# Kernel tuning notes

Hardware: AMD Instinct MI355X
Metric: run time of the kernel (lower is better)

Reference implementation:

```python
import math
import jax, jax.numpy as jnp
import numpy as np

B, L, S, H, E, D = 2, 2048, 2048, 16, 64, 64

def setup_inputs() -> dict:
    key = jax.random.key(0)
    k1, k2, k3, k4, k5 = jax.random.split(key, 5)
    return {
        "queries": jax.random.normal(k1, (B, L, H, E), dtype=jnp.float32),
        "keys": jax.random.normal(k2, (B, S, H, E), dtype=jnp.float32),
        "values": jax.random.normal(k3, (B, S, H, D), dtype=jnp.float32),
        "tau": jax.random.uniform(k4, (B, 1), dtype=jnp.float32),
        "delta": jax.random.normal(k5, (B, S), dtype=jnp.float32),
        "attn_mask": jnp.zeros((1,), dtype=jnp.bool_),
    }

def reference(queries, keys, values, tau, delta, attn_mask):
    # queries: [B,L,H,E], keys: [B,S,H,E], values: [B,S,H,D]
    # tau: [B,1] -> [B,1,1,1]; delta: [B,S] -> [B,1,1,S]
    # mask_flag=False, so attn_mask is unused. Dropout is identity at eval.
    E_ = queries.shape[-1]
    scale = 1.0 / math.sqrt(E_)
    scores = jnp.einsum('blhe,bshe->bhls', queries, keys)  # [B,H,L,S]
    scores = scores * tau[:, None, None, :]                # de-stationary scale
    scores = scores + delta[:, None, None, :]              # de-stationary shift
    A = jax.nn.softmax(scale * scores, axis=-1)            # [B,H,L,S]
    V = jnp.einsum('bhls,bshd->blhd', A, values)           # [B,L,H,D]
    return V
```

## Files before the change

### kernel.cpp

```cpp
#include <hip/hip_runtime.h>


#define Bb 2
#define Ll 2048
#define Ss 2048
#define Hh 16
#define Ee 64
#define Dd 64
#define KV 64

typedef _Float16 f16x8 __attribute__((ext_vector_type(8)));
typedef _Float16 f16x4 __attribute__((ext_vector_type(4)));
typedef __fp16 fp16x2 __attribute__((ext_vector_type(2)));
typedef float f32x4 __attribute__((ext_vector_type(4)));

union Pk2 { fp16x2 h; unsigned u; };
union PackU { unsigned u[4]; f16x8 v; };

#define GLDS(gp, lp) __builtin_amdgcn_global_load_lds( \
    (const __attribute__((address_space(1))) void*)(gp), \
    (__attribute__((address_space(3))) void*)(lp), 16, 0, 0)

__global__ __launch_bounds__(256)
void prepass_k(const float* __restrict__ K, _Float16* __restrict__ K16,
               const float* __restrict__ delta, float* __restrict__ delta2)
{
    const unsigned v = blockIdx.x * 256 + threadIdx.x;
    const unsigned e4 = v & 15;
    const unsigned h  = (v >> 4) & 15;
    const unsigned s  = (v >> 8) & (Ss - 1);
    const unsigned b  = v >> 19;
    const f32x4 src = ((const f32x4*)K)[v];
    f16x4 t;
    t[0] = (_Float16)src[0]; t[1] = (_Float16)src[1];
    t[2] = (_Float16)src[2]; t[3] = (_Float16)src[3];
    ((f16x4*)K16)[(((size_t)(b * Hh + h) * Ss + s) * 16) + e4] = t;
    if (v < (Bb * Ss) / 4) {
        f32x4 dd = ((const f32x4*)delta)[v];
        ((f32x4*)delta2)[v] = (f32x4){0.125f * dd[0], 0.125f * dd[1],
                                      0.125f * dd[2], 0.125f * dd[3]};
    }
}

__global__ __launch_bounds__(256)
void prepass_v(const float* __restrict__ V, _Float16* __restrict__ VT16)
{
    __shared__ _Float16 TL[64][66];
    const int tid  = threadIdx.x;
    const int wave = tid >> 6;
    const int lane = tid & 63;
    const int bh = blockIdx.y;
    const int b  = bh >> 4;
    const int h  = bh & 15;
    const int s0 = blockIdx.x * 64;

    #pragma unroll
    for (int rr = 0; rr < 16; ++rr) {
        const int row = wave * 16 + rr;
        TL[row][lane] = (_Float16)V[((size_t)(b * Ss + s0 + row) * Hh + h) * Dd + lane];
    }
    __syncthreads();
    const int d  = tid >> 2;
    const int sq = (tid & 3) * 16;
    union { _Float16 h[16]; f16x8 v[2]; } tmp;
    #pragma unroll
    for (int i = 0; i < 16; ++i) tmp.h[i] = TL[sq + i][d];
    f16x8* dp = (f16x8*)(VT16 + ((size_t)(b * Hh + h) * Dd + d) * Ss + s0 + sq);
    dp[0] = tmp.v[0];
    dp[1] = tmp.v[1];
}

__global__ __launch_bounds__(256)
void dsattn_fwd_v4(const float* __restrict__ Q, const _Float16* __restrict__ K16,
                   const _Float16* __restrict__ VT16, const float* __restrict__ tau,
                   const float* __restrict__ delta2, float* __restrict__ out)
{
    extern __shared__ __align__(16) unsigned char smem[];

    const int tid  = threadIdx.x;
    const int wave = tid >> 6;
    const int lane = tid & 63;
    const int lq   = lane & 15;
    const int g    = lane >> 4;

    const int bh = blockIdx.y;
    const int b  = bh >> 4;
    const int h  = bh & 15;
    const int q0 = blockIdx.x * 128;
    const int qw = q0 + wave * 32;

    const float alpha = 0.125f * tau[b];

    f16x8 aq[2][2];
    #pragma unroll
    for (int qg = 0; qg < 2; ++qg) {
        const float* qp = Q + (((size_t)b * Ll + qw + qg * 16 + lq) * Hh + h) * Ee;
        #pragma unroll
        for (int es = 0; es < 2; ++es) {
            const float* p = qp + es * 32 + g * 8;
            f16x8 t;
            #pragma unroll
            for (int j = 0; j < 8; ++j) t[j] = (_Float16)p[j];
            aq[qg][es] = t;
        }
    }

    f32x4 osum[2][4];
    #pragma unroll
    for (int qg = 0; qg < 2; ++qg)
        #pragma unroll
        for (int i = 0; i < 4; ++i) osum[qg][i] = (f32x4){0.f, 0.f, 0.f, 0.f};
    float m_run[2] = {-1e30f, -1e30f};
    float l_run[2] = {0.0f, 0.0f};

    const unsigned char* kb  = (const unsigned char*)(K16 + (size_t)(b * Hh + h) * Ss * Ee);
    const unsigned char* vtb = (const unsigned char*)(VT16 + (size_t)(b * Hh + h) * Dd * Ss);
    const float* d2b = delta2 + (size_t)b * Ss;

    const int row0  = tid >> 3;
    const int slotS = (tid & 7) ^ (row0 & 7);

    {
        unsigned char* kw = smem + wave * 1024;
        unsigned char* vw = smem + 8192 + wave * 1024;
        GLDS(kb + (size_t)row0 * 128 + slotS * 16,        kw);
        GLDS(kb + (size_t)(row0 + 32) * 128 + slotS * 16, kw + 4096);
        GLDS(vtb + (size_t)row0 * (Ss * 2) + slotS * 16,        vw);
        GLDS(vtb + (size_t)(row0 + 32) * (Ss * 2) + slotS * 16, vw + 4096);
    }
    f32x4 dcur[4], dnxt[4];
    #pragma unroll
    for (int t = 0; t < 4; ++t)
        dcur[t] = *(const f32x4*)(d2b + t * 16 + 4 * g);
    __syncthreads();

    const int srcA = lq + 32 * (g & 1);
    const int srcB = srcA + 16;
    const bool gh = (g >> 1);

    int cur = 0;
    for (int sb = 0; sb < Ss; sb += KV) {
        const int nb = (sb + KV < Ss);
        if (nb) {
            unsigned char* kw = smem + (cur ^ 1) * 16384 + wave * 1024;
            unsigned char* vw = kw + 8192;
            const int sn = sb + KV;
            GLDS(kb + (size_t)(sn + row0) * 128 + slotS * 16,        kw);
            GLDS(kb + (size_t)(sn + row0 + 32) * 128 + slotS * 16,   kw + 4096);
            GLDS(vtb + (size_t)row0 * (Ss * 2) + sn * 2 + slotS * 16,        vw);
            GLDS(vtb + (size_t)(row0 + 32) * (Ss * 2) + sn * 2 + slotS * 16, vw + 4096);
        }
        {
            const int sn = nb ? sb + KV : sb;
            #pragma unroll
            for (int t = 0; t < 4; ++t)
                dnxt[t] = *(const f32x4*)(d2b + sn + t * 16 + 4 * g);
        }

        const unsigned char* Ksm = smem + cur * 16384;
        const unsigned char* Vsm = Ksm + 8192;

        f32x4 c4[2][4];
        #pragma unroll
        for (int qg = 0; qg < 2; ++qg)
            #pragma unroll
            for (int t = 0; t < 4; ++t) c4[qg][t] = (f32x4){0.f, 0.f, 0.f, 0.f};
        __builtin_amdgcn_s_setprio(1);
        #pragma unroll
        for (int t = 0; t < 4; ++t) {
            const int srow = t * 16 + lq;
            #pragma unroll
            for (int es = 0; es < 2; ++es) {
                const int slot = (es * 4 + g) ^ (srow & 7);
                f16x8 ak = *(const f16x8*)(Ksm + srow * 128 + slot * 16);
                c4[0][t] = __builtin_amdgcn_mfma_f32_16x16x32_f16(ak, aq[0][es], c4[0][t], 0, 0, 0);
                c4[1][t] = __builtin_amdgcn_mfma_f32_16x16x32_f16(ak, aq[1][es], c4[1][t], 0, 0, 0);
            }
        }
        __builtin_amdgcn_s_setprio(0);

        PackU bp[2][2];
        #pragma unroll
        for (int qg = 0; qg < 2; ++qg) {
            float p[16];
            float tmax = -1e30f;
            #pragma unroll
            for (int t = 0; t < 4; ++t)
                #pragma unroll
                for (int j = 0; j < 4; ++j) {
                    float z = fmaf(alpha, c4[qg][t][j], dcur[t][j]);
                    p[t * 4 + j] = z;
                    tmax = fmaxf(tmax, z);
                }
            tmax = fmaxf(tmax, __shfl_xor(tmax, 16));
            tmax = fmaxf(tmax, __shfl_xor(tmax, 32));
            if (!__all(tmax <= m_run[qg] + 8.0f)) {
                const float m_new = fmaxf(m_run[qg], tmax);
                const float corr  = __expf(m_run[qg] - m_new);
                l_run[qg] *= corr;
                #pragma unroll
                for (int dt = 0; dt < 4; ++dt)
                    #pragma unroll
                    for (int j = 0; j < 4; ++j)
                        osum[qg][dt][j] *= corr;
                m_run[qg] = m_new;
            }
            float psum = 0.f;
            #pragma unroll
            for (int i = 0; i < 16; ++i) { p[i] = __expf(p[i] - m_run[qg]); psum += p[i]; }
            psum += __shfl_xor(psum, 16);
            psum += __shfl_xor(psum, 32);
            l_run[qg] += psum;

            unsigned pk[8];
            #pragma unroll
            for (int t = 0; t < 4; ++t) {
                Pk2 u0, u1;
                u0.h = __builtin_amdgcn_cvt_pkrtz(p[4 * t], p[4 * t + 1]);
                u1.h = __builtin_amdgcn_cvt_pkrtz(p[4 * t + 2], p[4 * t + 3]);
                pk[t * 2] = u0.u;
                pk[t * 2 + 1] = u1.u;
            }
            #pragma unroll
            for (int ks = 0; ks < 2; ++ks) {
                unsigned a0 = __shfl(pk[ks * 4 + 0], srcA), a1 = __shfl(pk[ks * 4 + 1], srcA);
                unsigned a2 = __shfl(pk[ks * 4 + 2], srcA), a3 = __shfl(pk[ks * 4 + 3], srcA);
                unsigned b0 = __shfl(pk[ks * 4 + 0], srcB), b1 = __shfl(pk[ks * 4 + 1], srcB);
                unsigned b2 = __shfl(pk[ks * 4 + 2], srcB), b3 = __shfl(pk[ks * 4 + 3], srcB);
                bp[qg][ks].u[0] = gh ? a2 : a0;
                bp[qg][ks].u[1] = gh ? a3 : a1;
                bp[qg][ks].u[2] = gh ? b2 : b0;
                bp[qg][ks].u[3] = gh ? b3 : b1;
            }
        }

        __builtin_amdgcn_s_setprio(1);
        #pragma unroll
        for (int ks = 0; ks < 2; ++ks)
            #pragma unroll
            for (int dt = 0; dt < 4; ++dt) {
                const int vrow = dt * 16 + lq;
                const int slot = (ks * 4 + g) ^ (vrow & 7);
                f16x8 av = *(const f16x8*)(Vsm + vrow * 128 + slot * 16);
                osum[0][dt] = __builtin_amdgcn_mfma_f32_16x16x32_f16(av, bp[0][ks].v, osum[0][dt], 0, 0, 0);
                osum[1][dt] = __builtin_amdgcn_mfma_f32_16x16x32_f16(av, bp[1][ks].v, osum[1][dt], 0, 0, 0);
            }
        __builtin_amdgcn_s_setprio(0);

        __syncthreads();
        cur ^= 1;
        #pragma unroll
        for (int t = 0; t < 4; ++t) dcur[t] = dnxt[t];
    }

    float (*Osm)[32][68] = (float (*)[32][68])smem;
    #pragma unroll
    for (int qg = 0; qg < 2; ++qg) {
        const float inv = 1.0f / l_run[qg];
        #pragma unroll
        for (int dt = 0; dt < 4; ++dt)
            #pragma unroll
            for (int j = 0; j < 4; ++j)
                Osm[wave][qg * 16 + lq][dt * 16 + 4 * g + j] = osum[qg][dt][j] * inv;
    }
    __syncthreads();
    {
        float* ob = out + (((size_t)b * Ll + qw) * Hh + h) * Dd;
        #pragma unroll
        for (int r = 0; r < 32; ++r)
            ob[(size_t)r * (Hh * Dd) + lane] = Osm[wave][r][lane];
    }
}

__global__ __launch_bounds__(256)
void dsattn_fwd(const float* __restrict__ Q, const float* __restrict__ K,
                const float* __restrict__ V, const float* __restrict__ tau,
                const float* __restrict__ delta, float* __restrict__ out)
{
    __shared__ __align__(16) unsigned char Ksm[32 * 128];
    __shared__ __align__(16) unsigned char VTsm[64 * 80];
    __shared__ float dsm[32];
    __shared__ float Osm[4][16][68];

    const int tid  = threadIdx.x;
    const int wave = tid >> 6;
    const int lane = tid & 63;
    const int lq   = lane & 15;
    const int g    = lane >> 4;

    const int bh = blockIdx.y;
    const int b  = bh >> 4;
    const int h  = bh & 15;
    const int q0 = blockIdx.x * 64;

    const float alpha = 0.125f * tau[b];

    f16x8 aq[2];
    {
        const float* qp = Q + (((long)b * Ll + q0 + wave * 16 + lq) * Hh + h) * Ee;
        #pragma unroll
        for (int es = 0; es < 2; ++es) {
            const float* p = qp + es * 32 + g * 8;
            f16x8 t;
            #pragma unroll
            for (int j = 0; j < 8; ++j) t[j] = (_Float16)p[j];
            aq[es] = t;
        }
    }

    f32x4 osum[4];
    #pragma unroll
    for (int i = 0; i < 4; ++i) osum[i] = (f32x4){0.f, 0.f, 0.f, 0.f};
    float m_run = -1e30f, l_run = 0.0f;

    const float* kb = K + ((long)b * Ss * Hh + h) * Ee;
    const float* vb = V + ((long)b * Ss * Hh + h) * Dd;
    const float* db = delta + (long)b * Ss;

    const int kr    = tid >> 3;
    const int kc    = (tid & 7) * 8;
    const int kslot = (((tid & 7) ^ (kr & 7)) * 16);
    const int vd    = tid & 63;
    const int vsh   = tid >> 6;

    for (int sb = 0; sb < Ss; sb += 32) {
        __syncthreads();
        {
            const float* src = kb + (long)(sb + kr) * (Hh * Ee) + kc;
            f16x8 t;
            #pragma unroll
            for (int j = 0; j < 8; ++j) t[j] = (_Float16)src[j];
            *(f16x8*)(Ksm + kr * 128 + kslot) = t;
        }
        {
            const float* src = vb + (long)(sb + vsh * 8) * (Hh * Dd) + vd;
            f16x8 t;
            #pragma unroll
            for (int j = 0; j < 8; ++j) t[j] = (_Float16)src[j * (Hh * Dd)];
            *(f16x8*)(VTsm + vd * 80 + vsh * 16) = t;
        }
        if (tid < 32) dsm[tid] = 0.125f * db[sb + tid];
        __syncthreads();

        float p[8];
        float tmax = -1e30f;
        #pragma unroll
        for (int t = 0; t < 2; ++t) {
            f32x4 c = (f32x4){0.f, 0.f, 0.f, 0.f};
            #pragma unroll
            for (int es = 0; es < 2; ++es) {
                const int srow = t * 16 + lq;
                const int slot = ((es * 4 + g) ^ (srow & 7)) * 16;
                f16x8 ak = *(const f16x8*)(Ksm + srow * 128 + slot);
                c = __builtin_amdgcn_mfma_f32_16x16x32_f16(ak, aq[es], c, 0, 0, 0);
            }
            #pragma unroll
            for (int j = 0; j < 4; ++j) {
                float z = alpha * c[j] + dsm[t * 16 + 4 * g + j];
                p[t * 4 + j] = z;
                tmax = fmaxf(tmax, z);
            }
        }
        tmax = fmaxf(tmax, __shfl_xor(tmax, 16));
        tmax = fmaxf(tmax, __shfl_xor(tmax, 32));
        const float m_new = fmaxf(m_run, tmax);
        const float corr  = __expf(m_run - m_new);
        float psum = 0.f;
        #pragma unroll
        for (int i = 0; i < 8; ++i) { p[i] = __expf(p[i] - m_new); psum += p[i]; }
        psum += __shfl_xor(psum, 16);
        psum += __shfl_xor(psum, 32);
        l_run = l_run * corr + psum;
        m_run = m_new;
        #pragma unroll
        for (int dt = 0; dt < 4; ++dt)
            #pragma unroll
            for (int j = 0; j < 4; ++j)
                osum[dt][j] *= corr;

        Pk2 u00, u01, u10, u11;
        u00.h = __builtin_amdgcn_cvt_pkrtz(p[0], p[1]);
        u01.h = __builtin_amdgcn_cvt_pkrtz(p[2], p[3]);
        u10.h = __builtin_amdgcn_cvt_pkrtz(p[4], p[5]);
        u11.h = __builtin_amdgcn_cvt_pkrtz(p[6], p[7]);
        const int srcA = lq + 32 * (g & 1);
        const int srcB = srcA + 16;
        unsigned a00 = __shfl(u00.u, srcA), a01 = __shfl(u01.u, srcA);
        unsigned a10 = __shfl(u10.u, srcA), a11 = __shfl(u11.u, srcA);
        unsigned b00 = __shfl(u00.u, srcB), b01 = __shfl(u01.u, srcB);
        unsigned b10 = __shfl(u10.u, srcB), b11 = __shfl(u11.u, srcB);
        const bool hi = (g >= 2);
        PackU bp;
        bp.u[0] = hi ? a10 : a00;
        bp.u[1] = hi ? a11 : a01;
        bp.u[2] = hi ? b10 : b00;
        bp.u[3] = hi ? b11 : b01;

        #pragma unroll
        for (int dt = 0; dt < 4; ++dt) {
            f16x8 av = *(const f16x8*)(VTsm + (dt * 16 + lq) * 80 + g * 16);
            osum[dt] = __builtin_amdgcn_mfma_f32_16x16x32_f16(av, bp.v, osum[dt], 0, 0, 0);
        }
    }

    const float inv = 1.0f / l_run;
    #pragma unroll
    for (int dt = 0; dt < 4; ++dt)
        #pragma unroll
        for (int j = 0; j < 4; ++j)
            Osm[wave][lq][dt * 16 + 4 * g + j] = osum[dt][j] * inv;
    __syncthreads();
    {
        float* ob = out + (((long)b * Ll + q0 + wave * 16) * Hh + h) * Dd;
        #pragma unroll
        for (int r = 0; r < 16; ++r)
            ob[(long)r * (Hh * Dd) + lane] = Osm[wave][r][lane];
    }
}

extern "C" void kernel_launch(void* const* d_in, const int* in_sizes, int n_in,
                              void* d_out, int out_size, void* d_ws, size_t ws_size,
                              hipStream_t stream) {
    const float* Q     = (const float*)d_in[0];
    const float* K     = (const float*)d_in[1];
    const float* V     = (const float*)d_in[2];
    const float* tau   = (const float*)d_in[3];
    const float* delta = (const float*)d_in[4];
    float* out = (float*)d_out;

    const size_t elems = (size_t)Bb * Hh * Ss * Ee;
    const size_t need  = elems * 2 * 2 + (size_t)Bb * Ss * 4;

    if (ws_size >= need) {
        _Float16* K16    = (_Float16*)d_ws;
        _Float16* VT16   = K16 + elems;
        float*    delta2 = (float*)(VT16 + elems);
        hipLaunchKernelGGL(prepass_k, dim3(elems / 4 / 256), dim3(256), 0, stream,
                           K, K16, delta, delta2);
        hipLaunchKernelGGL(prepass_v, dim3(Ss / 64, Bb * Hh), dim3(256), 0, stream, V, VT16);
        hipLaunchKernelGGL(dsattn_fwd_v4, dim3(Ll / 128, Bb * Hh), dim3(256), 34816, stream,
                           Q, K16, VT16, tau, delta2, out);
    } else {
        hipLaunchKernelGGL(dsattn_fwd, dim3(Ll / 64, Bb * Hh), dim3(256), 0, stream,
                           Q, K, V, tau, delta, out);
    }
}
```

Measured before the change: 95.27 us.

## Split KV sequence across two wave groups per block with in-block softmax merge

Doubles the block to 512 threads and has each half of the waves process half of the key/value sequence for the same 128 queries, each with its own double-buffered LDS staging. The second half writes its partial output, running max and running sum to shared memory, and the first half merges them with the standard log-sum-exp rescaling before the output is stored. This is meant to raise the number of waves in flight, since the grid is only 512 blocks, and to shorten each wave's serial KV loop. The cost is 64KB of LDS per block, which limits blocks per CU, plus extra merge and synchronisation work at the end.

```diff
diff --git a/kernel.cpp b/kernel.cpp
--- a/kernel.cpp
+++ b/kernel.cpp
@@ -70,8 +70,8 @@
     dp[1] = tmp.v[1];
 }
 
-__global__ __launch_bounds__(256)
-void dsattn_fwd_v4(const float* __restrict__ Q, const _Float16* __restrict__ K16,
+__global__ __launch_bounds__(512)
+void dsattn_fwd_v5(const float* __restrict__ Q, const _Float16* __restrict__ K16,
                    const _Float16* __restrict__ VT16, const float* __restrict__ tau,
                    const float* __restrict__ delta2, float* __restrict__ out)
 {
@@ -79,15 +79,18 @@
 
     const int tid  = threadIdx.x;
     const int wave = tid >> 6;
+    const int half = wave >> 2;
+    const int wq   = wave & 3;
     const int lane = tid & 63;
     const int lq   = lane & 15;
     const int g    = lane >> 4;
+    const int tid_h = tid & 255;
 
     const int bh = blockIdx.y;
     const int b  = bh >> 4;
     const int h  = bh & 15;
     const int q0 = blockIdx.x * 128;
-    const int qw = q0 + wave * 32;
+    const int qw = q0 + wq * 32;
 
     const float alpha = 0.125f * tau[b];
 
@@ -117,21 +120,23 @@
     const unsigned char* vtb = (const unsigned char*)(VT16 + (size_t)(b * Hh + h) * Dd * Ss);
     const float* d2b = delta2 + (size_t)b * Ss;
 
-    const int row0  = tid >> 3;
-    const int slotS = (tid & 7) ^ (row0 & 7);
+    const int row0  = tid_h >> 3;
+    const int slotS = (tid_h & 7) ^ (row0 & 7);
+    unsigned char* stBase = smem + half * 32768;
+    const int sBase = half * (Ss / 2);
 
     {
-        unsigned char* kw = smem + wave * 1024;
-        unsigned char* vw = smem + 8192 + wave * 1024;
-        GLDS(kb + (size_t)row0 * 128 + slotS * 16,        kw);
-        GLDS(kb + (size_t)(row0 + 32) * 128 + slotS * 16, kw + 4096);
-        GLDS(vtb + (size_t)row0 * (Ss * 2) + slotS * 16,        vw);
-        GLDS(vtb + (size_t)(row0 + 32) * (Ss * 2) + slotS * 16, vw + 4096);
+        unsigned char* kw = stBase + wq * 1024;
+        unsigned char* vw = stBase + 8192 + wq * 1024;
+        GLDS(kb + (size_t)(sBase + row0) * 128 + slotS * 16,        kw);
+        GLDS(kb + (size_t)(sBase + row0 + 32) * 128 + slotS * 16,   kw + 4096);
+        GLDS(vtb + (size_t)row0 * (Ss * 2) + sBase * 2 + slotS * 16,        vw);
+        GLDS(vtb + (size_t)(row0 + 32) * (Ss * 2) + sBase * 2 + slotS * 16, vw + 4096);
     }
     f32x4 dcur[4], dnxt[4];
     #pragma unroll
     for (int t = 0; t < 4; ++t)
-        dcur[t] = *(const f32x4*)(d2b + t * 16 + 4 * g);
+        dcur[t] = *(const f32x4*)(d2b + sBase + t * 16 + 4 * g);
     __syncthreads();
 
     const int srcA = lq + 32 * (g & 1);
@@ -139,10 +144,11 @@
     const bool gh = (g >> 1);
 
     int cur = 0;
-    for (int sb = 0; sb < Ss; sb += KV) {
-        const int nb = (sb + KV < Ss);
+    for (int it = 0; it < Ss / 2 / KV; ++it) {
+        const int sb = sBase + it * KV;
+        const int nb = (it + 1 < Ss / 2 / KV);
         if (nb) {
-            unsigned char* kw = smem + (cur ^ 1) * 16384 + wave * 1024;
+            unsigned char* kw = stBase + (cur ^ 1) * 16384 + wq * 1024;
             unsigned char* vw = kw + 8192;
             const int sn = sb + KV;
             GLDS(kb + (size_t)(sn + row0) * 128 + slotS * 16,        kw);
@@ -157,7 +163,7 @@
                 dnxt[t] = *(const f32x4*)(d2b + sn + t * 16 + 4 * g);
         }
 
-        const unsigned char* Ksm = smem + cur * 16384;
+        const unsigned char* Ksm = stBase + cur * 16384;
         const unsigned char* Vsm = Ksm + 8192;
 
         f32x4 c4[2][4];
@@ -253,22 +259,55 @@
         for (int t = 0; t < 4; ++t) dcur[t] = dnxt[t];
     }
 
-    float (*Osm)[32][68] = (float (*)[32][68])smem;
-    #pragma unroll
-    for (int qg = 0; qg < 2; ++qg) {
-        const float inv = 1.0f / l_run[qg];
-        #pragma unroll
-        for (int dt = 0; dt < 4; ++dt)
-            #pragma unroll
-            for (int j = 0; j < 4; ++j)
-                Osm[wave][qg * 16 + lq][dt * 16 + 4 * g + j] = osum[qg][dt][j] * inv;
+    float (*Part)[2][16][68] = (float (*)[2][16][68])smem;
+    if (half == 1) {
+        #pragma unroll
+        for (int qg = 0; qg < 2; ++qg) {
+            #pragma unroll
+            for (int dt = 0; dt < 4; ++dt)
+                *(f32x4*)&Part[wq][qg][lq][dt * 16 + 4 * g] = osum[qg][dt];
+            if (g == 0) {
+                Part[wq][qg][lq][64] = m_run[qg];
+                Part[wq][qg][lq][65] = l_run[qg];
+            }
+        }
+    }
+    __syncthreads();
+    if (half == 0) {
+        #pragma unroll
+        for (int qg = 0; qg < 2; ++qg) {
+            const float m1 = Part[wq][qg][lq][64];
+            const float l1 = Part[wq][qg][lq][65];
+            const float m  = fmaxf(m_run[qg], m1);
+            const float s0 = __expf(m_run[qg] - m);
+            const float s1 = __expf(m1 - m);
+            const float inv = 1.0f / (l_run[qg] * s0 + l1 * s1);
+            #pragma unroll
+            for (int dt = 0; dt < 4; ++dt) {
+                f32x4 p1 = *(const f32x4*)&Part[wq][qg][lq][dt * 16 + 4 * g];
+                #pragma unroll
+                for (int j = 0; j < 4; ++j)
+                    osum[qg][dt][j] = (osum[qg][dt][j] * s0 + p1[j] * s1) * inv;
+            }
+        }
+    }
+    __syncthreads();
+    float (*Osm)[68] = (float (*)[68])smem;
+    if (half == 0) {
+        #pragma unroll
+        for (int qg = 0; qg < 2; ++qg)
+            #pragma unroll
+            for (int dt = 0; dt < 4; ++dt)
+                *(f32x4*)&Osm[wq * 32 + qg * 16 + lq][dt * 16 + 4 * g] = osum[qg][dt];
     }
     __syncthreads();
     {
-        float* ob = out + (((size_t)b * Ll + qw) * Hh + h) * Dd;
-        #pragma unroll
-        for (int r = 0; r < 32; ++r)
-            ob[(size_t)r * (Hh * Dd) + lane] = Osm[wave][r][lane];
+        float* ob = out + (((size_t)b * Ll + q0) * Hh + h) * Dd;
+        #pragma unroll
+        for (int i = 0; i < 16; ++i) {
+            const int r = wave * 16 + i;
+            ob[(size_t)r * (Hh * Dd) + lane] = Osm[r][lane];
+        }
     }
 }
 
@@ -438,7 +477,7 @@
         hipLaunchKernelGGL(prepass_k, dim3(elems / 4 / 256), dim3(256), 0, stream,
                            K, K16, delta, delta2);
         hipLaunchKernelGGL(prepass_v, dim3(Ss / 64, Bb * Hh), dim3(256), 0, stream, V, VT16);
-        hipLaunchKernelGGL(dsattn_fwd_v4, dim3(Ll / 128, Bb * Hh), dim3(256), 34816, stream,
+        hipLaunchKernelGGL(dsattn_fwd_v5, dim3(Ll / 128, Bb * Hh), dim3(512), 65536, stream,
                            Q, K16, VT16, tau, delta2, out);
     } else {
         hipLaunchKernelGGL(dsattn_fwd, dim3(Ll / 64, Bb * Hh), dim3(256), 0, stream,
```

Result: no change. 94.24 us (-1.1%).
